# Optimization experiments

Hardware: AMD Instinct MI355X
Metric: run time of the kernel (lower is better)

Reference implementation:

```python
import jax, jax.numpy as jnp
import numpy as np

B, S, D, H = 2, 2048, 1024, 16
HD = D // H  # head_dim = 64
SCALE = HD ** -0.5


def setup_inputs() -> dict:
    key = jax.random.key(0)
    k1, k2, k3 = jax.random.split(key, 3)
    src = jax.random.normal(k1, (B, S, D), dtype=jnp.float32)
    w_qkv = jax.random.normal(k2, (D, 3 * D), dtype=jnp.float32) * (D ** -0.5)
    b_qkv = jax.random.normal(k3, (3 * D,), dtype=jnp.float32) * 0.02
    return {"src": src, "w_qkv": w_qkv, "b_qkv": b_qkv}


def reference(src, w_qkv, b_qkv):
    # qkv projection: [B,S,3D]
    qkv = src @ w_qkv + b_qkv
    q, k, v = jnp.split(qkv, 3, axis=-1)
    # [B,S,D] -> [B,H,S,HD]
    def heads(x):
        return x.reshape(B, S, H, HD).transpose(0, 2, 1, 3)
    q, k, v = heads(q), heads(k), heads(v)
    # scaled dot-product attention (note: original scales AFTER q@k.T)
    attn = jnp.einsum('bhqd,bhkd->bhqk', q, k) * SCALE
    attn = jax.nn.softmax(attn, axis=-1)
    out = jnp.einsum('bhqk,bhkd->bhqd', attn, v)  # [B,H,S,HD]
    return out.transpose(0, 2, 1, 3).reshape(B, S, D)
```

## Files before the change

kernel.cpp:

```cpp
#include <hip/hip_runtime.h>
#include <hip/hip_bf16.h>

typedef short short8 __attribute__((ext_vector_type(8)));
typedef float f32x4 __attribute__((ext_vector_type(4)));
typedef float f32x16 __attribute__((ext_vector_type(16)));
typedef __hip_bfloat16 bf16;


__device__ __forceinline__ void glds16(const void* g, void* l) {
  __builtin_amdgcn_global_load_lds((const __attribute__((address_space(1))) unsigned int*)g,
                                   (__attribute__((address_space(3))) unsigned int*)l, 16, 0, 0);
}

__device__ __forceinline__ uint pk2(float a, float b) {
  union { bf16 h2[2]; uint u; } pk;
  pk.h2[0] = __float2bfloat16(a);
  pk.h2[1] = __float2bfloat16(b);
  return pk.u;
}

__global__ __launch_bounds__(256) void prep_kernel(const float4* __restrict__ in,
                                                   bf16* __restrict__ src_bf,
                                                   const float* __restrict__ w,
                                                   bf16* __restrict__ wt) {
  __shared__ float tile[64][33];
  const int bid = blockIdx.x;
  if (bid < 4096) {
    int i = bid * 256 + threadIdx.x;
    float4 v = in[i];
    union { bf16 h[4]; uint2 u; } pk;
    pk.h[0] = __float2bfloat16(v.x);
    pk.h[1] = __float2bfloat16(v.y);
    pk.h[2] = __float2bfloat16(v.z);
    pk.h[3] = __float2bfloat16(v.w);
    *(uint2*)(src_bf + (size_t)i * 4) = pk.u;
  } else {
    int id = bid - 4096;
    int x0 = (id % 96) * 32;
    int y0 = (id / 96) * 64;
    int tx = threadIdx.x & 31, ty = threadIdx.x >> 5;
#pragma unroll
    for (int i = 0; i < 8; i++) {
      int y = ty + i * 8;
      tile[y][tx] = w[(size_t)(y0 + y) * 3072 + x0 + tx];
    }
    __syncthreads();
#pragma unroll
    for (int j = 0; j < 4; j++) {
      int r = ty + j * 8;
      uint u = pk2(tile[2 * tx][r], tile[2 * tx + 1][r]);
      *(uint*)&wt[(size_t)(x0 + r) * 1024 + y0 + 2 * tx] = u;
    }
  }
}

__global__ __launch_bounds__(256) void qkv_gemm_kernel(
    const bf16* __restrict__ A, const bf16* __restrict__ Bt,
    const float* __restrict__ bias,
    bf16* __restrict__ q_ws, bf16* __restrict__ k_ws, bf16* __restrict__ vt_ws) {
  __shared__ alignas(16) char AB[32768];
  const int tid = threadIdx.x;
  const int lane = tid & 63, wid = tid >> 6;
  const int lr = lane & 15, lg = lane >> 4;
  const int wm = wid >> 1, wn = wid & 1;
  const int lin = blockIdx.y * 32 + blockIdx.x;
  const int xcd = lin & 7, idx = lin >> 3;
  const int bx = xcd * 4 + (idx & 3);
  const int by = idx >> 2;
  const int m0 = bx * 128, n0 = by * 128;

  const f32x4 z4 = {0.f, 0.f, 0.f, 0.f};
  f32x4 acc[4][4];
#pragma unroll
  for (int m = 0; m < 4; m++)
#pragma unroll
    for (int n = 0; n < 4; n++) acc[m][n] = z4;

  const int srow = lane >> 3;
  const int sseg = (lane & 7) ^ srow;
  const char* Ag = (const char*)A + (size_t)(m0 + wid * 32 + srow) * 2048 + sseg * 16;
  const char* Bg = (const char*)Bt + (size_t)(n0 + wid * 32 + srow) * 2048 + sseg * 16;
  char* Al = AB + wid * 4096;
  char* Bl = AB + 16384 + wid * 4096;
  const int xora = (lr & 7) << 4;

  for (int kt = 0; kt < 16; kt++) {
    __syncthreads();
#pragma unroll
    for (int c = 0; c < 4; c++) {
      glds16(Ag + (size_t)kt * 128 + c * 16384, Al + c * 1024);
      glds16(Bg + (size_t)kt * 128 + c * 16384, Bl + c * 1024);
    }
    asm volatile("s_waitcnt vmcnt(0)" ::: "memory");
    __syncthreads();
#pragma unroll
    for (int g = 0; g < 2; g++) {
      short8 af[4], bfr[4];
#pragma unroll
      for (int m = 0; m < 4; m++)
        af[m] = *(const short8*)(AB + (wm * 64 + m * 16 + lr) * 128 +
                                 ((g * 64 + lg * 16) ^ xora));
#pragma unroll
      for (int n = 0; n < 4; n++)
        bfr[n] = *(const short8*)(AB + 16384 + (wn * 64 + n * 16 + lr) * 128 +
                                  ((g * 64 + lg * 16) ^ xora));
#pragma unroll
      for (int m = 0; m < 4; m++)
#pragma unroll
        for (int n = 0; n < 4; n++)
          acc[m][n] = __builtin_amdgcn_mfma_f32_16x16x32_bf16(af[m], bfr[n], acc[m][n], 0, 0, 0);
    }
  }

  const int which = n0 >> 10;
  const float scl = (which == 0) ? 0.18033688f : 1.0f;
#pragma unroll
  for (int m = 0; m < 4; m++) {
    int row = m0 + wm * 64 + m * 16 + lg * 4;
    int b = row >> 11;
    int ss0 = row & 2047;
#pragma unroll
    for (int n = 0; n < 4; n++) {
      int col = n0 + wn * 64 + n * 16 + lr;
      int d = col & 1023;
      int h = d >> 6, hd = d & 63;
      size_t bh = (size_t)(b * 16 + h);
      float bv = bias[col];
      if (which == 2) {
        union { bf16 h4[4]; uint2 u; } pk;
#pragma unroll
        for (int r = 0; r < 4; r++) pk.h4[r] = __float2bfloat16(acc[m][n][r] + bv);
        *(uint2*)&vt_ws[(bh * 64 + hd) * 2048 + ss0] = pk.u;
      } else {
        bf16* dst = (which == 0) ? q_ws : k_ws;
#pragma unroll
        for (int r = 0; r < 4; r++)
          dst[(bh * 2048 + (ss0 + r)) * 64 + hd] = __float2bfloat16((acc[m][n][r] + bv) * scl);
      }
    }
  }
}

#define KPERM(p) (((p) & ~31) | ((p) & 3) | ((((p) >> 2) & 1) << 3) | \
                  ((((p) >> 3) & 1) << 4) | ((((p) >> 4) & 1) << 2))

__global__ __launch_bounds__(512) void attn9_kernel(
    const bf16* __restrict__ q_ws, const bf16* __restrict__ k_ws,
    const bf16* __restrict__ vt_ws, float* __restrict__ out) {
  __shared__ alignas(16) char smem[131072];
  const int tid = threadIdx.x;
  const int lane = tid & 63, wid = tid >> 6;
  const int lq = lane & 31, hi = lane >> 5;
  const int hi16 = hi * 16;
  const int xorv = (lq & 7) << 4;

  const int f = blockIdx.x;
  const int bh = (f & 7) * 4 + ((f >> 3) & 3);
  const int qb = f >> 5;
  const int b = bh >> 4, h = bh & 15;
  const int q0 = qb * 256 + wid * 32;

  short8 qf[4];
  {
    const bf16* qrow = q_ws + ((size_t)bh * 2048 + q0 + lq) * 64;
#pragma unroll
    for (int s = 0; s < 4; s++) qf[s] = *(const short8*)(qrow + s * 16 + hi * 8);
  }

  const int l8 = lane >> 3;
  const int segk = (lane & 7) ^ l8;
  const int p0 = wid * 16 + l8;
  const int p1 = p0 + 8;
  const char* kgl0 = (const char*)k_ws + (size_t)bh * 262144 +
                     (size_t)KPERM(p0) * 128 + segk * 16;
  const char* kgl1 = (const char*)k_ws + (size_t)bh * 262144 +
                     (size_t)KPERM(p1) * 128 + segk * 16;
  const int l16 = lane >> 4;
  const int d0v = (wid * 2 + 0) * 4 + l16;
  const int d1v = (wid * 2 + 1) * 4 + l16;
  const char* vg0 = (const char*)vt_ws + (size_t)bh * 262144 + (size_t)d0v * 4096 +
                    (((lane & 15) ^ (d0v & 15)) << 4);
  const char* vg1 = (const char*)vt_ws + (size_t)bh * 262144 + (size_t)d1v * 4096 +
                    (((lane & 15) ^ (d1v & 15)) << 4);

  f32x16 o0a, o0b, o1a, o1b, lacc;
#pragma unroll
  for (int r = 0; r < 16; r++) {
    o0a[r] = 0.f; o0b[r] = 0.f; o1a[r] = 0.f; o1b[r] = 0.f; lacc[r] = 0.f;
  }

#pragma unroll
  for (int p = 0; p < 2; p++) {
    glds16(kgl0 + (size_t)p * 16384, smem + p * 16384 + wid * 2048);
    glds16(kgl1 + (size_t)p * 16384, smem + p * 16384 + wid * 2048 + 1024);
    glds16(vg0 + (size_t)p * 256, smem + 65536 + p * 16384 + wid * 2048);
    glds16(vg1 + (size_t)p * 256, smem + 65536 + p * 16384 + wid * 2048 + 1024);
  }
  asm volatile("s_waitcnt vmcnt(0)" ::: "memory");
  __builtin_amdgcn_s_barrier();

  for (int kt = 0; kt < 16; ++kt) {
    const int kb_off = (kt & 3) * 16384;
    const int vb_off = 65536 + (kt & 3) * 16384;
    if (kt + 2 < 16) {
      const int nb = ((kt + 2) & 3) * 16384;
      glds16(kgl0 + (size_t)(kt + 2) * 16384, smem + nb + wid * 2048);
      glds16(kgl1 + (size_t)(kt + 2) * 16384, smem + nb + wid * 2048 + 1024);
      glds16(vg0 + (size_t)(kt + 2) * 256, smem + 65536 + nb + wid * 2048);
      glds16(vg1 + (size_t)(kt + 2) * 256, smem + 65536 + nb + wid * 2048 + 1024);
    }

    f32x16 s0, s1, s2, s3;
#pragma unroll
    for (int r = 0; r < 16; r++) { s0[r] = 0.f; s1[r] = 0.f; s2[r] = 0.f; s3[r] = 0.f; }
#pragma unroll
    for (int st = 0; st < 4; st++) {
      const int doff = (st * 32 + hi16) ^ xorv;
      short8 ka = *(const short8*)(smem + kb_off + lq * 128 + doff);
      short8 kb = *(const short8*)(smem + kb_off + (lq + 32) * 128 + doff);
      short8 kc = *(const short8*)(smem + kb_off + (lq + 64) * 128 + doff);
      short8 kd = *(const short8*)(smem + kb_off + (lq + 96) * 128 + doff);
      __builtin_amdgcn_s_setprio(1);
      s0 = __builtin_amdgcn_mfma_f32_32x32x16_bf16(ka, qf[st], s0, 0, 0, 0);
      s1 = __builtin_amdgcn_mfma_f32_32x32x16_bf16(kb, qf[st], s1, 0, 0, 0);
      s2 = __builtin_amdgcn_mfma_f32_32x32x16_bf16(kc, qf[st], s2, 0, 0, 0);
      s3 = __builtin_amdgcn_mfma_f32_32x32x16_bf16(kd, qf[st], s3, 0, 0, 0);
      __builtin_amdgcn_s_setprio(0);
    }

#pragma unroll
    for (int r = 0; r < 16; r++) {
      s0[r] = __builtin_amdgcn_exp2f(s0[r]);
      s1[r] = __builtin_amdgcn_exp2f(s1[r]);
      s2[r] = __builtin_amdgcn_exp2f(s2[r]);
      s3[r] = __builtin_amdgcn_exp2f(s3[r]);
    }
#pragma unroll
    for (int r = 0; r < 16; r++)
      lacc[r] += (s0[r] + s1[r]) + (s2[r] + s3[r]);

#define PV_KB(S, KB, OA, OB)                                                     \
  {                                                                              \
    union { uint u[4]; short8 s8; } ua, ub;                                      \
    ua.u[0] = pk2(S[0], S[1]);   ua.u[1] = pk2(S[2], S[3]);                      \
    ua.u[2] = pk2(S[8], S[9]);   ua.u[3] = pk2(S[10], S[11]);                    \
    ub.u[0] = pk2(S[4], S[5]);   ub.u[1] = pk2(S[6], S[7]);                      \
    ub.u[2] = pk2(S[12], S[13]); ub.u[3] = pk2(S[14], S[15]);                    \
    const int c0 = (((KB) * 4 + hi) ^ (lq & 15)) << 4;                           \
    const int c1 = (((KB) * 4 + 2 + hi) ^ (lq & 15)) << 4;                       \
    short8 va0 = *(const short8*)(smem + vb_off + lq * 256 + c0);                \
    short8 va1 = *(const short8*)(smem + vb_off + (lq + 32) * 256 + c0);         \
    short8 vb0 = *(const short8*)(smem + vb_off + lq * 256 + c1);                \
    short8 vb1 = *(const short8*)(smem + vb_off + (lq + 32) * 256 + c1);         \
    __builtin_amdgcn_s_setprio(1);                                               \
    OA = __builtin_amdgcn_mfma_f32_32x32x16_bf16(va0, ua.s8, OA, 0, 0, 0);       \
    OB = __builtin_amdgcn_mfma_f32_32x32x16_bf16(va1, ua.s8, OB, 0, 0, 0);       \
    OA = __builtin_amdgcn_mfma_f32_32x32x16_bf16(vb0, ub.s8, OA, 0, 0, 0);       \
    OB = __builtin_amdgcn_mfma_f32_32x32x16_bf16(vb1, ub.s8, OB, 0, 0, 0);       \
    __builtin_amdgcn_s_setprio(0);                                               \
  }
    PV_KB(s0, 0, o0a, o1a)
    PV_KB(s1, 1, o0b, o1b)
    PV_KB(s2, 2, o0a, o1a)
    PV_KB(s3, 3, o0b, o1b)
#undef PV_KB

    if ((kt & 1) && kt < 15) {
      asm volatile("s_waitcnt vmcnt(0)" ::: "memory");
      __builtin_amdgcn_s_barrier();
    }
  }
  __syncthreads();

  float l;
  {
    float sm[8];
#pragma unroll
    for (int i = 0; i < 8; i++) sm[i] = lacc[i] + lacc[i + 8];
#pragma unroll
    for (int i = 0; i < 4; i++) sm[i] += sm[i + 4];
    l = (sm[0] + sm[1]) + (sm[2] + sm[3]);
    l += __shfl_xor(l, 32);
  }
  f32x16 o0, o1;
#pragma unroll
  for (int r = 0; r < 16; r++) { o0[r] = o0a[r] + o0b[r]; o1[r] = o1a[r] + o1b[r]; }
  float* ep = (float*)(smem) + wid * 1024;
  const float invl = 1.f / l;
  const int eq = lane >> 1, eds = lane & 1;
  float* obase = out + ((size_t)b * 2048 + qb * 256 + wid * 32 + eq) * 1024 +
                 h * 64 + eds * 16;
#pragma unroll
  for (int db = 0; db < 2; db++) {
#pragma unroll
    for (int r = 0; r < 16; r++) {
      int d = (r & 3) + 8 * (r >> 2) + 4 * hi;
      float v = (db ? o1[r] : o0[r]) * invl;
      ep[lq * 32 + ((d + lq) & 31)] = v;
    }
#pragma unroll
    for (int c = 0; c < 4; c++) {
      float4 t;
      t.x = ep[eq * 32 + ((eds * 16 + 4 * c + 0 + eq) & 31)];
      t.y = ep[eq * 32 + ((eds * 16 + 4 * c + 1 + eq) & 31)];
      t.z = ep[eq * 32 + ((eds * 16 + 4 * c + 2 + eq) & 31)];
      t.w = ep[eq * 32 + ((eds * 16 + 4 * c + 3 + eq) & 31)];
      *(float4*)(obase + db * 32 + 4 * c) = t;
    }
  }
}

extern "C" void kernel_launch(void* const* d_in, const int* in_sizes, int n_in,
                              void* d_out, int out_size, void* d_ws, size_t ws_size,
                              hipStream_t stream) {
  (void)in_sizes; (void)n_in; (void)out_size; (void)ws_size;
  const float* src  = (const float*)d_in[0];
  const float* w    = (const float*)d_in[1];
  const float* bias = (const float*)d_in[2];
  float* out = (float*)d_out;

  char* ws = (char*)d_ws;
  bf16* src_bf = (bf16*)ws;
  bf16* wt_bf  = (bf16*)(ws + 8388608);
  bf16* q_ws   = (bf16*)(ws + 8388608 + 6291456);
  bf16* k_ws   = q_ws + 4194304;
  bf16* vt_ws  = k_ws + 4194304;

  prep_kernel<<<5632, 256, 0, stream>>>((const float4*)src, src_bf, w, wt_bf);
  qkv_gemm_kernel<<<dim3(32, 24), 256, 0, stream>>>(src_bf, wt_bf, bias, q_ws, k_ws, vt_ws);
  attn9_kernel<<<256, 512, 0, stream>>>(q_ws, k_ws, vt_ws, out);
}
```

Measured before the change: 89.74 us.

## Rewrite QKV GEMM as 256x256 tile, 8-wave double-buffered pipelined kernel

The QKV projection GEMM now uses 256x256 output tiles with 512 threads and a 128KB double-buffered LDS ring. Global-to-LDS loads for the next k-step are interleaved with the MFMA work on the current step, split into four phases. Each phase is fenced with s_barrier and uses s_setprio to raise priority around the MFMA blocks. This increases data reuse per tile and aims to hide load latency. The cost is one block per CU and only 192 blocks for the whole grid, plus a confusing redundant prologue load whose address arithmetic looks leftover.

```diff
diff --git a/kernel.cpp b/kernel.cpp
--- a/kernel.cpp
+++ b/kernel.cpp
@@ -54,69 +54,165 @@
   }
 }
 
-__global__ __launch_bounds__(256) void qkv_gemm_kernel(
+__global__ __launch_bounds__(512, 1) void qkv_gemm_kernel(
     const bf16* __restrict__ A, const bf16* __restrict__ Bt,
     const float* __restrict__ bias,
     bf16* __restrict__ q_ws, bf16* __restrict__ k_ws, bf16* __restrict__ vt_ws) {
-  __shared__ alignas(16) char AB[32768];
+  __shared__ alignas(16) char smem[131072];
   const int tid = threadIdx.x;
   const int lane = tid & 63, wid = tid >> 6;
   const int lr = lane & 15, lg = lane >> 4;
-  const int wm = wid >> 1, wn = wid & 1;
-  const int lin = blockIdx.y * 32 + blockIdx.x;
-  const int xcd = lin & 7, idx = lin >> 3;
-  const int bx = xcd * 4 + (idx & 3);
-  const int by = idx >> 2;
-  const int m0 = bx * 128, n0 = by * 128;
+  const int wm = wid >> 2, wn = wid & 3;
+
+  const int lin = blockIdx.x;
+  const int rem = (lin & 7) * 24 + (lin >> 3);
+  const int bx = rem & 15, by = rem >> 4;
+  const int m0 = bx * 256, n0 = by * 256;
+
+  const int t0 = tid;
+  const int r0s = t0 >> 3, s0s = (t0 & 7) ^ (r0s & 7);
+  const int t1 = tid + 512;
+  const int r1s = t1 >> 3, s1s = (t1 & 7) ^ (r1s & 7);
+  const bf16* As[2][2];
+  const bf16* Bs[2][2];
+#pragma unroll
+  for (int h = 0; h < 2; h++) {
+    As[h][0] = A + (size_t)(m0 + h * 128 + r0s) * 1024 + s0s * 8;
+    As[h][1] = A + (size_t)(m0 + h * 128 + r1s) * 1024 + s1s * 8;
+    Bs[h][0] = Bt + (size_t)(n0 + h * 128 + r0s) * 1024 + s0s * 8;
+    Bs[h][1] = Bt + (size_t)(n0 + h * 128 + r1s) * 1024 + s1s * 8;
+  }
 
   const f32x4 z4 = {0.f, 0.f, 0.f, 0.f};
-  f32x4 acc[4][4];
-#pragma unroll
-  for (int m = 0; m < 4; m++)
+  f32x4 acc[8][4];
+#pragma unroll
+  for (int m = 0; m < 8; m++)
 #pragma unroll
     for (int n = 0; n < 4; n++) acc[m][n] = z4;
 
-  const int srow = lane >> 3;
-  const int sseg = (lane & 7) ^ srow;
-  const char* Ag = (const char*)A + (size_t)(m0 + wid * 32 + srow) * 2048 + sseg * 16;
-  const char* Bg = (const char*)Bt + (size_t)(n0 + wid * 32 + srow) * 2048 + sseg * 16;
-  char* Al = AB + wid * 4096;
-  char* Bl = AB + 16384 + wid * 4096;
-  const int xora = (lr & 7) << 4;
-
-  for (int kt = 0; kt < 16; kt++) {
-    __syncthreads();
-#pragma unroll
-    for (int c = 0; c < 4; c++) {
-      glds16(Ag + (size_t)kt * 128 + c * 16384, Al + c * 1024);
-      glds16(Bg + (size_t)kt * 128 + c * 16384, Bl + c * 1024);
-    }
+  const int aoff = wm * 16384;
+  const int boff = 65536 + (wn >> 1) * 16384;
+  const int rBbase = (wn & 1) * 64;
+  const int fx = (lr & 7) << 4;
+
+#pragma unroll
+  for (int h = 0; h < 2; h++) {
+    glds16(As[h][0], smem + h * 16384 + tid * 16 - (tid & 7) * 16 + (s0s ^ (r0s & 7)) * 0 + (t0 * 16 - t0 * 16) + t0 * 16);
+  }
+  __builtin_amdgcn_s_barrier();
+#pragma unroll
+  for (int h = 0; h < 2; h++) {
+    glds16(As[h][0], smem + h * 16384 + t0 * 16);
+    glds16(As[h][1], smem + h * 16384 + 8192 + (t0 * 16));
+    glds16(Bs[h][0], smem + 65536 + h * 16384 + t0 * 16);
+    glds16(Bs[h][1], smem + 65536 + h * 16384 + 8192 + t0 * 16);
+  }
+  asm volatile("s_waitcnt vmcnt(0)" ::: "memory");
+  __builtin_amdgcn_s_barrier();
+
+  for (int t = 0; t < 16; ++t) {
+    const int cur = (t & 1) * 32768;
+    const int nxt = ((t + 1) & 1) * 32768;
+    const int stg = (t + 1) * 64;
+    short8 bfr0[4], bfr1[4], af[4];
+
+#pragma unroll
+    for (int n = 0; n < 4; n++) {
+      const int rB = rBbase + n * 16 + lr;
+      bfr0[n] = *(const short8*)(smem + boff + cur + rB * 128 + ((lg * 16) ^ fx));
+    }
+#pragma unroll
+    for (int m = 0; m < 4; m++) {
+      const int rA = m * 16 + lr;
+      af[m] = *(const short8*)(smem + aoff + cur + rA * 128 + ((lg * 16) ^ fx));
+    }
+    if (t < 15) {
+      glds16(As[0][0] + stg, smem + nxt + t0 * 16);
+      glds16(As[0][1] + stg, smem + nxt + 8192 + t0 * 16);
+    }
+    __builtin_amdgcn_s_barrier();
+    asm volatile("s_waitcnt lgkmcnt(0)" ::: "memory");
+    __builtin_amdgcn_s_setprio(1);
+#pragma unroll
+    for (int m = 0; m < 4; m++)
+#pragma unroll
+      for (int n = 0; n < 4; n++)
+        acc[m][n] = __builtin_amdgcn_mfma_f32_16x16x32_bf16(af[m], bfr0[n], acc[m][n], 0, 0, 0);
+    __builtin_amdgcn_s_setprio(0);
+    __builtin_amdgcn_s_barrier();
+
+#pragma unroll
+    for (int m = 0; m < 4; m++) {
+      const int rA = (m + 4) * 16 + lr;
+      af[m] = *(const short8*)(smem + aoff + cur + rA * 128 + ((lg * 16) ^ fx));
+    }
+    if (t < 15) {
+      glds16(As[1][0] + stg, smem + nxt + 16384 + t0 * 16);
+      glds16(As[1][1] + stg, smem + nxt + 16384 + 8192 + t0 * 16);
+    }
+    __builtin_amdgcn_s_barrier();
+    asm volatile("s_waitcnt lgkmcnt(0)" ::: "memory");
+    __builtin_amdgcn_s_setprio(1);
+#pragma unroll
+    for (int m = 0; m < 4; m++)
+#pragma unroll
+      for (int n = 0; n < 4; n++)
+        acc[m + 4][n] = __builtin_amdgcn_mfma_f32_16x16x32_bf16(af[m], bfr0[n], acc[m + 4][n], 0, 0, 0);
+    __builtin_amdgcn_s_setprio(0);
+    __builtin_amdgcn_s_barrier();
+
+#pragma unroll
+    for (int n = 0; n < 4; n++) {
+      const int rB = rBbase + n * 16 + lr;
+      bfr1[n] = *(const short8*)(smem + boff + cur + rB * 128 + ((64 + lg * 16) ^ fx));
+    }
+#pragma unroll
+    for (int m = 0; m < 4; m++) {
+      const int rA = m * 16 + lr;
+      af[m] = *(const short8*)(smem + aoff + cur + rA * 128 + ((64 + lg * 16) ^ fx));
+    }
+    if (t < 15) {
+      glds16(Bs[0][0] + stg, smem + 65536 + nxt + t0 * 16);
+      glds16(Bs[0][1] + stg, smem + 65536 + nxt + 8192 + t0 * 16);
+    }
+    __builtin_amdgcn_s_barrier();
+    asm volatile("s_waitcnt lgkmcnt(0)" ::: "memory");
+    __builtin_amdgcn_s_setprio(1);
+#pragma unroll
+    for (int m = 0; m < 4; m++)
+#pragma unroll
+      for (int n = 0; n < 4; n++)
+        acc[m][n] = __builtin_amdgcn_mfma_f32_16x16x32_bf16(af[m], bfr1[n], acc[m][n], 0, 0, 0);
+    __builtin_amdgcn_s_setprio(0);
+    __builtin_amdgcn_s_barrier();
+
+#pragma unroll
+    for (int m = 0; m < 4; m++) {
+      const int rA = (m + 4) * 16 + lr;
+      af[m] = *(const short8*)(smem + aoff + cur + rA * 128 + ((64 + lg * 16) ^ fx));
+    }
+    if (t < 15) {
+      glds16(Bs[1][0] + stg, smem + 65536 + nxt + 16384 + t0 * 16);
+      glds16(Bs[1][1] + stg, smem + 65536 + nxt + 16384 + 8192 + t0 * 16);
+    }
+    __builtin_amdgcn_s_barrier();
+    asm volatile("s_waitcnt lgkmcnt(0)" ::: "memory");
+    __builtin_amdgcn_s_setprio(1);
+#pragma unroll
+    for (int m = 0; m < 4; m++)
+#pragma unroll
+      for (int n = 0; n < 4; n++)
+        acc[m + 4][n] = __builtin_amdgcn_mfma_f32_16x16x32_bf16(af[m], bfr1[n], acc[m + 4][n], 0, 0, 0);
+    __builtin_amdgcn_s_setprio(0);
     asm volatile("s_waitcnt vmcnt(0)" ::: "memory");
-    __syncthreads();
-#pragma unroll
-    for (int g = 0; g < 2; g++) {
-      short8 af[4], bfr[4];
-#pragma unroll
-      for (int m = 0; m < 4; m++)
-        af[m] = *(const short8*)(AB + (wm * 64 + m * 16 + lr) * 128 +
-                                 ((g * 64 + lg * 16) ^ xora));
-#pragma unroll
-      for (int n = 0; n < 4; n++)
-        bfr[n] = *(const short8*)(AB + 16384 + (wn * 64 + n * 16 + lr) * 128 +
-                                  ((g * 64 + lg * 16) ^ xora));
-#pragma unroll
-      for (int m = 0; m < 4; m++)
-#pragma unroll
-        for (int n = 0; n < 4; n++)
-          acc[m][n] = __builtin_amdgcn_mfma_f32_16x16x32_bf16(af[m], bfr[n], acc[m][n], 0, 0, 0);
-    }
+    __builtin_amdgcn_s_barrier();
   }
 
   const int which = n0 >> 10;
   const float scl = (which == 0) ? 0.18033688f : 1.0f;
 #pragma unroll
-  for (int m = 0; m < 4; m++) {
-    int row = m0 + wm * 64 + m * 16 + lg * 4;
+  for (int m = 0; m < 8; m++) {
+    int row = m0 + wm * 128 + m * 16 + lg * 4;
     int b = row >> 11;
     int ss0 = row & 2047;
 #pragma unroll
@@ -327,6 +423,6 @@
   bf16* vt_ws  = k_ws + 4194304;
 
   prep_kernel<<<5632, 256, 0, stream>>>((const float4*)src, src_bf, w, wt_bf);
-  qkv_gemm_kernel<<<dim3(32, 24), 256, 0, stream>>>(src_bf, wt_bf, bias, q_ws, k_ws, vt_ws);
+  qkv_gemm_kernel<<<192, 512, 0, stream>>>(src_bf, wt_bf, bias, q_ws, k_ws, vt_ws);
   attn9_kernel<<<256, 512, 0, stream>>>(q_ws, k_ws, vt_ws, out);
 }
```

Result: slower. 93.63 us (+4.3%).
